# Optimization experiments

Hardware: AMD Instinct MI355X
Metric: run time of the kernel (lower is better)

## Reference

```python
import jax, jax.numpy as jnp
import numpy as np

RADIUS = 0.3      # extents/2, extents = radius_scale*6*particle_radius = 4*6*0.025 = 0.6
KSIZE = 4         # kernel_size [4,4,4]
KMAX = 80         # padded neighbor count
N = 50000
BOX = 5.2         # box side -> ~40 neighbors within RADIUS on average
CIN = 3
COUT = 3
_PI = 3.14159265358979323846


def _build_neighbors(pos, radius, kmax):
    # fixed-radius search (L2), ignore_query_point=True, padded to kmax per row
    n = pos.shape[0]
    r2 = radius * radius
    sq = (pos * pos).sum(1)
    idx = np.zeros((n, kmax), np.int32)
    msk = np.zeros((n, kmax), np.bool_)
    ch = 2500
    for s in range(0, n, ch):
        e = min(s + ch, n)
        d2 = sq[s:e, None] + sq[None, :] - 2.0 * (pos[s:e] @ pos.T)
        d2[np.arange(e - s), np.arange(s, e)] = np.inf  # radius_search_ignore_query_points
        rows, cols = np.nonzero(d2 < r2)
        starts = np.searchsorted(rows, np.arange(e - s))
        slot = np.arange(len(rows)) - starts[rows]
        keep = slot < kmax
        idx[rows[keep] + s, slot[keep]] = cols[keep]
        msk[rows[keep] + s, slot[keep]] = True
    return idx, msk


def setup_inputs():
    key = jax.random.key(0)
    k1, k2, k3 = jax.random.split(key, 3)
    pos = jax.random.uniform(k1, (N, 3), jnp.float32) * BOX
    vel = jax.random.normal(k2, (N, 3), jnp.float32)
    # keras 'uniform' initializer: U(-0.05, 0.05)
    kernel = jax.random.uniform(k3, (KSIZE, KSIZE, KSIZE, CIN, COUT), jnp.float32, -0.05, 0.05)
    nidx, nmask = _build_neighbors(np.asarray(pos), RADIUS, KMAX)
    return {"pos": pos, "vel": vel, "kernel": kernel,
            "neighbor_idx": jnp.asarray(nidx), "neighbor_mask": jnp.asarray(nmask)}


def _ball_to_cube_volume_preserving(u):
    # Open3D CoordinateTransformation.h: MapSphereToCylinder then MapCylinderToCube
    eps = 1e-12
    x, y, z = u[..., 0], u[..., 1], u[..., 2]
    sq = x * x + y * y + z * z
    norm = jnp.sqrt(jnp.maximum(sq, eps))
    sq_xy = x * x + y * y
    # sphere -> cylinder
    top = (1.25 * z * z) > sq_xy
    s_top = jnp.sqrt(3.0 * norm / (norm + jnp.abs(z)))
    s_side = norm / jnp.sqrt(jnp.maximum(sq_xy, eps))
    x1 = jnp.where(top, x * s_top, x * s_side)
    y1 = jnp.where(top, y * s_top, y * s_side)
    z1 = jnp.where(top, jnp.sign(z) * norm, 1.5 * z)
    small = sq < eps
    x1 = jnp.where(small, x, x1)
    y1 = jnp.where(small, y, y1)
    z1 = jnp.where(small, z, z1)
    # cylinder -> cube (equal-area disc->square on xy)
    sq_xy1 = x1 * x1 + y1 * y1
    norm_xy = jnp.sqrt(jnp.maximum(sq_xy1, eps))
    xbig = jnp.abs(y1) <= jnp.abs(x1)
    sx = jnp.sign(x1) * norm_xy
    sy = jnp.sign(y1) * norm_xy
    safe_x = jnp.where(jnp.abs(x1) > eps, x1, 1.0)
    safe_y = jnp.where(jnp.abs(y1) > eps, y1, 1.0)
    x2 = jnp.where(xbig, sx, sy * (4.0 / _PI) * jnp.arctan(x1 / safe_y))
    y2 = jnp.where(xbig, sx * (4.0 / _PI) * jnp.arctan(y1 / safe_x), sy)
    small_xy = sq_xy1 < eps
    x2 = jnp.where(small_xy, x1, x2)
    y2 = jnp.where(small_xy, y1, y2)
    return x2, y2, z1


def _grid_coords(c):
    # align_corners=True: [-1,1] -> [0, KSIZE-1]; 'linear' interpolation clamps to border
    t = jnp.clip((c + 1.0) * (0.5 * (KSIZE - 1)), 0.0, KSIZE - 1.0)
    t0 = jnp.floor(t)
    i0 = t0.astype(jnp.int32)
    i1 = jnp.minimum(i0 + 1, KSIZE - 1)
    f = t - t0
    return (i0, i1), (1.0 - f, f)


def _cconv(pos, vel, kernel, neighbor_idx, neighbor_mask):
    n = pos.shape[0]
    rel = pos[neighbor_idx] - pos[:, None, :]              # [N,K,3]
    d2 = jnp.sum(rel * rel, -1)
    # window_poly6 on squared distance normalized by radius^2
    imp = jnp.clip((1.0 - d2 / (RADIUS * RADIUS)) ** 3, 0.0, 1.0)
    imp = imp * neighbor_mask.astype(vel.dtype)
    cx, cy, cz = _ball_to_cube_volume_preserving(rel / RADIUS)
    (xi0, xi1), (wx0, wx1) = _grid_coords(cx)
    (yi0, yi1), (wy0, wy1) = _grid_coords(cy)
    (zi0, zi1), (wz0, wz1) = _grid_coords(cz)
    phi = vel[neighbor_idx] * imp[..., None]               # [N,K,Cin]
    rows = jnp.arange(n)[:, None]
    # accumulate window*trilinear-weighted features into the 64 filter taps,
    # then contract once with the flattened kernel (math identical to per-pair
    # interp(W) @ feat since everything is linear)
    A = jnp.zeros((n, KSIZE * KSIZE * KSIZE, vel.shape[1]), vel.dtype)
    for zi, wz in ((zi0, wz0), (zi1, wz1)):
        for yi, wy in ((yi0, wy0), (yi1, wy1)):
            for xi, wx in ((xi0, wx0), (xi1, wx1)):
                corner = (zi * KSIZE + yi) * KSIZE + xi
                A = A.at[rows, corner].add((wz * wy * wx)[..., None] * phi)
    Wflat = kernel.reshape(KSIZE * KSIZE * KSIZE, kernel.shape[3], kernel.shape[4])
    return jnp.einsum('ngi,gio->no', A, Wflat)        # [N, COUT]


def reference(pos, vel, kernel, neighbor_idx, neighbor_mask):
    return _cconv(pos, vel, kernel, neighbor_idx, neighbor_mask)
```

## Files before the change

### kernel.cpp

```cpp
#include <hip/hip_runtime.h>
#include <math.h>

#define N_PART 50000
#define KMAX 80
#define KS 4
#define LPP 16

typedef __attribute__((ext_vector_type(8))) _Float16 h8;
typedef __attribute__((ext_vector_type(2))) _Float16 h2;

__device__ __forceinline__ float atan_poly(float t) {
    float t2 = t * t;
    float p = -0.01172120f;
    p = p * t2 + 0.05265332f;
    p = p * t2 - 0.11643287f;
    p = p * t2 + 0.19354346f;
    p = p * t2 - 0.33262347f;
    p = p * t2 + 0.99997726f;
    return t * p;
}

template <typename MT>
__device__ __forceinline__ int prefix_count(const MT* __restrict__ nmask, int base, int sub) {
    int lc = 0; bool more = true;
    #pragma unroll
    for (int i = 0; i < 5; ++i) {
        bool t = nmask[base + sub * 5 + i] != 0;
        lc += (more && t) ? 1 : 0;
        more = more && t;
    }
    bool full = (lc == 5);
    unsigned long long nb = __ballot(!full);
    int wl  = threadIdx.x & 63;
    int grp = wl >> 4;
    unsigned int gb = (unsigned int)((nb >> (16 * grp)) & 0xFFFFull);
    if (gb == 0) return KMAX;
    int fi  = __ffs(gb) - 1;
    int flc = __shfl(lc, (grp << 4) + fi, 64);
    return fi * 5 + flc;
}

struct PV { float px, py, pz, ux, uy, uz; };

__device__ __forceinline__ void load_pv(const float* __restrict__ pos,
                                        const float* __restrict__ vel,
                                        int i, PV& v) {
    v.px = pos[3*i];  v.py = pos[3*i+1];  v.pz = pos[3*i+2];
    v.ux = vel[3*i];  v.uy = vel[3*i+1];  v.uz = vel[3*i+2];
}

__device__ __forceinline__ void pair_contrib(
    const PV& n, float cpx, float cpy, float cpz,
    const _Float16* __restrict__ WsH, const float* __restrict__ Ws8,
    float& acc0, float& acc1, float& acc2)
{
    const float inv_r = 1.0f / 0.3f;
    const float eps   = 1e-12f;
    const float FOUR_OVER_PI = 1.27323954473516268615f;

    float rx = (n.px - cpx) * inv_r;
    float ry = (n.py - cpy) * inv_r;
    float rz = (n.pz - cpz) * inv_r;

    float sq = rx * rx + ry * ry + rz * rz;

    float t1  = 1.0f - sq;
    float imp = fmaxf(t1 * t1 * t1, 0.0f);

    float norm   = sqrtf(fmaxf(sq, eps));
    float sq_xy  = rx * rx + ry * ry;
    bool  top    = (1.25f * rz * rz) > sq_xy;
    float rsq_xy = __builtin_amdgcn_rsqf(fmaxf(sq_xy, eps));
    float s_top  = sqrtf(3.0f * norm * __builtin_amdgcn_rcpf(norm + fabsf(rz)));
    float s_side = norm * rsq_xy;
    float s  = top ? s_top : s_side;
    float z1 = top ? copysignf(norm, rz) : 1.5f * rz;

    float nxy = top ? (sq_xy * rsq_xy * s_top) : norm;
    bool  xb  = fabsf(ry) <= fabsf(rx);
    float num = xb ? ry : rx;
    float den = xb ? rx : ry;
    float sden = (fabsf(den) > eps) ? den : 1.0f;
    float t    = num * __builtin_amdgcn_rcpf(sden);
    float at   = atan_poly(t);
    float sd   = copysignf(nxy, den);
    float u    = sd * FOUR_OVER_PI * at;
    float x2   = xb ? sd : u;
    float y2   = xb ? u  : sd;

    float tx = fminf(fmaxf((x2 + 1.0f) * 1.5f, 0.0f), 3.0f);
    float ty = fminf(fmaxf((y2 + 1.0f) * 1.5f, 0.0f), 3.0f);
    float tz = fminf(fmaxf((z1 + 1.0f) * 1.5f, 0.0f), 3.0f);
    float fx0 = floorf(tx), fy0 = floorf(ty), fz0 = floorf(tz);
    int xi0 = (int)fx0, yi0 = (int)fy0, zi0 = (int)fz0;
    int xi1 = min(xi0 + 1, KS - 1);
    int yi1 = min(yi0 + 1, KS - 1);
    int zi1 = min(zi0 + 1, KS - 1);
    float wx1 = tx - fx0, wx0 = 1.0f - wx1;
    float wy1 = ty - fy0, wy0 = 1.0f - wy1;
    float wz1 = tz - fz0, wz0 = 1.0f - wz1;

    int   zia[2] = { zi0 << 4, zi1 << 4 };  float wza[2] = { wz0, wz1 };
    int   yia[2] = { yi0 << 2, yi1 << 2 };  float wya[2] = { wy0, wy1 };
    int   xia[2] = { xi0, xi1 };            float wxa[2] = { wx0, wx1 };

    h2 M01 = (h2)(_Float16)0.0f;
    h2 M23 = (h2)(_Float16)0.0f;
    h2 M45 = (h2)(_Float16)0.0f;
    h2 M67 = (h2)(_Float16)0.0f;
    float m8 = 0.0f;

    #pragma unroll
    for (int cz = 0; cz < 2; ++cz) {
        #pragma unroll
        for (int cy = 0; cy < 2; ++cy) {
            float wzy = wza[cz] * wya[cy];
            int   czy = zia[cz] + yia[cy];
            #pragma unroll
            for (int cx = 0; cx < 2; ++cx) {
                int corner = czy + xia[cx];
                h8 wv = *(const h8*)&WsH[corner << 3];
                float wf = wzy * wxa[cx];
                _Float16 wh = (_Float16)wf;
                h2 ww = { wh, wh };
                M01 += ww * __builtin_shufflevector(wv, wv, 0, 1);
                M23 += ww * __builtin_shufflevector(wv, wv, 2, 3);
                M45 += ww * __builtin_shufflevector(wv, wv, 4, 5);
                M67 += ww * __builtin_shufflevector(wv, wv, 6, 7);
                m8  += wf * Ws8[corner];
            }
        }
    }

    float m0 = (float)M01[0], m1 = (float)M01[1];
    float m2 = (float)M23[0], m3 = (float)M23[1];
    float m4 = (float)M45[0], m5 = (float)M45[1];
    float m6 = (float)M67[0], m7 = (float)M67[1];
    float s0 = n.ux * m0 + n.uy * m3 + n.uz * m6;
    float s1 = n.ux * m1 + n.uy * m4 + n.uz * m7;
    float s2 = n.ux * m2 + n.uy * m5 + n.uz * m8;
    acc0 += imp * s0;
    acc1 += imp * s1;
    acc2 += imp * s2;
}

__global__ __launch_bounds__(256) void cconv_kernel(
    const float* __restrict__ pos,
    const float* __restrict__ vel,
    const float* __restrict__ Wg,
    const int* __restrict__ nidx,
    const void* __restrict__ nmask,
    float* __restrict__ out)
{
    __shared__ _Float16 WsH[64 * 8];
    __shared__ float    Ws8[64];
    for (int t = threadIdx.x; t < 64 * 8; t += blockDim.x) {
        int g = t >> 3, r = t & 7;
        WsH[t] = (_Float16)Wg[g * 9 + r];
    }
    for (int t = threadIdx.x; t < 64; t += blockDim.x)
        Ws8[t] = Wg[t * 9 + 8];
    __syncthreads();

    int gid = blockIdx.x * blockDim.x + threadIdx.x;
    int p   = gid >> 4;
    int sub = gid & 15;
    if (p >= N_PART) return;

    const int base = p * KMAX;

    int idxs[5];
    #pragma unroll
    for (int m = 0; m < 5; ++m)
        idxs[m] = nidx[base + sub + (m << 4)];

    bool byteMask;
    {
        const unsigned* mw = (const unsigned*)nmask;
        int lane = threadIdx.x & 63;
        bool big = false;
        #pragma unroll
        for (int i = 0; i < 8; ++i)
            big |= (mw[lane + 64 * i] > 1u);
        byteMask = (__ballot(big) != 0ULL);
    }

    float cpx = pos[3 * p], cpy = pos[3 * p + 1], cpz = pos[3 * p + 2];

    int cnt;
    if (byteMask) cnt = prefix_count<unsigned char>((const unsigned char*)nmask, base, sub);
    else          cnt = prefix_count<int>((const int*)nmask, base, sub);

    PV A, An;
    load_pv(pos, vel, idxs[0], A);

    float acc0 = 0.0f, acc1 = 0.0f, acc2 = 0.0f;

    int m = 0;
    for (int k = sub; k < cnt; k += LPP) {
        int mn = min(m + 1, 4);
        load_pv(pos, vel, idxs[mn], An);

        pair_contrib(A, cpx, cpy, cpz, WsH, Ws8, acc0, acc1, acc2);

        A = An; ++m;
    }

    acc0 += __shfl_xor(acc0, 1); acc0 += __shfl_xor(acc0, 2);
    acc0 += __shfl_xor(acc0, 4); acc0 += __shfl_xor(acc0, 8);
    acc1 += __shfl_xor(acc1, 1); acc1 += __shfl_xor(acc1, 2);
    acc1 += __shfl_xor(acc1, 4); acc1 += __shfl_xor(acc1, 8);
    acc2 += __shfl_xor(acc2, 1); acc2 += __shfl_xor(acc2, 2);
    acc2 += __shfl_xor(acc2, 4); acc2 += __shfl_xor(acc2, 8);

    if (sub == 0) {
        out[p * 3 + 0] = acc0;
        out[p * 3 + 1] = acc1;
        out[p * 3 + 2] = acc2;
    }
}

extern "C" void kernel_launch(void* const* d_in, const int* in_sizes, int n_in,
                              void* d_out, int out_size, void* d_ws, size_t ws_size,
                              hipStream_t stream) {
    const float* pos   = (const float*)d_in[0];
    const float* vel   = (const float*)d_in[1];
    const float* Wg    = (const float*)d_in[2];
    const int*   nidx  = (const int*)d_in[3];
    const void*  nmask = d_in[4];
    float*       out   = (float*)d_out;

    int threads = 256;
    long long total = (long long)N_PART * LPP;
    int grid = (int)((total + threads - 1) / threads);
    cconv_kernel<<<grid, threads, 0, stream>>>(pos, vel, Wg, nidx, nmask, out);
}
```

Baseline: 29.16 us.

## Use 32 lanes per particle and count neighbors by mask popcount reduction

```diff
diff --git a/kernel.cpp b/kernel.cpp
--- a/kernel.cpp
+++ b/kernel.cpp
@@ -4,7 +4,7 @@
 #define N_PART 50000
 #define KMAX 80
 #define KS 4
-#define LPP 16
+#define LPP 32
 
 typedef __attribute__((ext_vector_type(8))) _Float16 h8;
 typedef __attribute__((ext_vector_type(2))) _Float16 h2;
@@ -20,26 +20,6 @@
     return t * p;
 }
 
-template <typename MT>
-__device__ __forceinline__ int prefix_count(const MT* __restrict__ nmask, int base, int sub) {
-    int lc = 0; bool more = true;
-    #pragma unroll
-    for (int i = 0; i < 5; ++i) {
-        bool t = nmask[base + sub * 5 + i] != 0;
-        lc += (more && t) ? 1 : 0;
-        more = more && t;
-    }
-    bool full = (lc == 5);
-    unsigned long long nb = __ballot(!full);
-    int wl  = threadIdx.x & 63;
-    int grp = wl >> 4;
-    unsigned int gb = (unsigned int)((nb >> (16 * grp)) & 0xFFFFull);
-    if (gb == 0) return KMAX;
-    int fi  = __ffs(gb) - 1;
-    int flc = __shfl(lc, (grp << 4) + fi, 64);
-    return fi * 5 + flc;
-}
-
 struct PV { float px, py, pz, ux, uy, uz; };
 
 __device__ __forceinline__ void load_pv(const float* __restrict__ pos,
@@ -72,8 +52,6 @@
     bool  top    = (1.25f * rz * rz) > sq_xy;
     float rsq_xy = __builtin_amdgcn_rsqf(fmaxf(sq_xy, eps));
     float s_top  = sqrtf(3.0f * norm * __builtin_amdgcn_rcpf(norm + fabsf(rz)));
-    float s_side = norm * rsq_xy;
-    float s  = top ? s_top : s_side;
     float z1 = top ? copysignf(norm, rz) : 1.5f * rz;
 
     float nxy = top ? (sq_xy * rsq_xy * s_top) : norm;
@@ -163,16 +141,15 @@
     __syncthreads();
 
     int gid = blockIdx.x * blockDim.x + threadIdx.x;
-    int p   = gid >> 4;
-    int sub = gid & 15;
-    if (p >= N_PART) return;
+    int p   = gid >> 5;
+    int sub = gid & 31;
 
     const int base = p * KMAX;
 
-    int idxs[5];
-    #pragma unroll
-    for (int m = 0; m < 5; ++m)
-        idxs[m] = nidx[base + sub + (m << 4)];
+    int idxs[3];
+    idxs[0] = nidx[base + sub];
+    idxs[1] = nidx[base + min(sub + 32, KMAX - 1)];
+    idxs[2] = nidx[base + min(sub + 64, KMAX - 1)];
 
     bool byteMask;
     {
@@ -187,9 +164,21 @@
 
     float cpx = pos[3 * p], cpy = pos[3 * p + 1], cpz = pos[3 * p + 2];
 
-    int cnt;
-    if (byteMask) cnt = prefix_count<unsigned char>((const unsigned char*)nmask, base, sub);
-    else          cnt = prefix_count<int>((const int*)nmask, base, sub);
+    int lc;
+    if (byteMask) {
+        const unsigned char* mb = (const unsigned char*)nmask;
+        lc  = (mb[base + sub]      != 0);
+        lc += (mb[base + sub + 32] != 0);
+        if (sub < 16) lc += (mb[base + sub + 64] != 0);
+    } else {
+        const int* mi = (const int*)nmask;
+        lc  = (mi[base + sub]      != 0);
+        lc += (mi[base + sub + 32] != 0);
+        if (sub < 16) lc += (mi[base + sub + 64] != 0);
+    }
+    lc += __shfl_xor(lc, 1);  lc += __shfl_xor(lc, 2);  lc += __shfl_xor(lc, 4);
+    lc += __shfl_xor(lc, 8);  lc += __shfl_xor(lc, 16);
+    const int cnt = lc;
 
     PV A, An;
     load_pv(pos, vel, idxs[0], A);
@@ -198,7 +187,7 @@
 
     int m = 0;
     for (int k = sub; k < cnt; k += LPP) {
-        int mn = min(m + 1, 4);
+        int mn = min(m + 1, 2);
         load_pv(pos, vel, idxs[mn], An);
 
         pair_contrib(A, cpx, cpy, cpz, WsH, Ws8, acc0, acc1, acc2);
@@ -206,12 +195,15 @@
         A = An; ++m;
     }
 
-    acc0 += __shfl_xor(acc0, 1); acc0 += __shfl_xor(acc0, 2);
-    acc0 += __shfl_xor(acc0, 4); acc0 += __shfl_xor(acc0, 8);
-    acc1 += __shfl_xor(acc1, 1); acc1 += __shfl_xor(acc1, 2);
-    acc1 += __shfl_xor(acc1, 4); acc1 += __shfl_xor(acc1, 8);
-    acc2 += __shfl_xor(acc2, 1); acc2 += __shfl_xor(acc2, 2);
-    acc2 += __shfl_xor(acc2, 4); acc2 += __shfl_xor(acc2, 8);
+    acc0 += __shfl_xor(acc0, 1);  acc0 += __shfl_xor(acc0, 2);
+    acc0 += __shfl_xor(acc0, 4);  acc0 += __shfl_xor(acc0, 8);
+    acc0 += __shfl_xor(acc0, 16);
+    acc1 += __shfl_xor(acc1, 1);  acc1 += __shfl_xor(acc1, 2);
+    acc1 += __shfl_xor(acc1, 4);  acc1 += __shfl_xor(acc1, 8);
+    acc1 += __shfl_xor(acc1, 16);
+    acc2 += __shfl_xor(acc2, 1);  acc2 += __shfl_xor(acc2, 2);
+    acc2 += __shfl_xor(acc2, 4);  acc2 += __shfl_xor(acc2, 8);
+    acc2 += __shfl_xor(acc2, 16);
 
     if (sub == 0) {
         out[p * 3 + 0] = acc0;
```

Result: slower. 31.18 us (+6.9%).
